# Kernel optimization log

Measured on AMD Instinct MI355X. Metric: run time of the kernel, lower is better.

## Reference

```python
import jax, jax.numpy as jnp
import numpy as np

B, N, H, NH = 2, 1024, 1024, 16  # batch, seq per branch, hidden, heads


def setup_inputs() -> dict:
    key = jax.random.key(0)
    k1, k2, k3, k4 = jax.random.split(key, 4)
    x = jax.random.normal(k1, (B, N, H), jnp.float32)
    x2 = jax.random.normal(k2, (B, N, H), jnp.float32)
    w_qkv = jax.random.normal(k3, (3 * H, H), jnp.float32) * 0.02  # nn.Linear(H, 3H), no bias
    w_out = jax.random.normal(k4, (H, H), jnp.float32) * 0.02
    b_out = jnp.zeros((H,), jnp.float32)
    return {"x": x, "x2": x2, "w_qkv": w_qkv, "w_out": w_out, "b_out": b_out, "num_heads": NH}


def _qkv_split(x, w_qkv, nh):
    # qkv Linear then Rearrange 'b n (qkv l d) -> qkv b l n d'
    b, n, h = x.shape
    d = h // nh
    qkv = x @ w_qkv.T                                    # [b, n, 3h]
    qkv = qkv.reshape(b, n, 3, nh, d).transpose(2, 0, 3, 1, 4)  # [3, b, nh, n, d]
    return qkv[0], qkv[1], qkv[2]


def reference(x, x2, w_qkv, w_out, b_out, num_heads):
    nh = num_heads
    d = x.shape[-1] // nh
    scale = float(d) ** -0.5
    q, k, v = _qkv_split(x, w_qkv, nh)
    q2, k2, v2 = _qkv_split(x2, w_qkv, nh)
    # cross-branch concat along seq dim
    q = jnp.concatenate([q, q2], axis=2)
    k = jnp.concatenate([k, k2], axis=2)
    v = jnp.concatenate([v, v2], axis=2)
    att = jax.nn.softmax(jnp.einsum('bhxd,bhyd->bhxy', q, k) * scale, axis=-1)  # [b,nh,2N,2N]
    o = jnp.einsum('bhxy,bhyd->bhxd', att, v)            # [b,nh,2N,d]
    o1, o2 = jnp.split(o, 2, axis=2)

    def proj(o):
        b, h, n, dd = o.shape
        o = o.transpose(0, 2, 1, 3).reshape(b, n, h * dd)  # 'b h l d -> b l (h d)'
        return o @ w_out.T + b_out

    return proj(o1), proj(o2)
```

## Files before the change

kernel.cpp:

```cpp
#include <hip/hip_runtime.h>
#include <hip/hip_bf16.h>

#define NB      2
#define NSEQ    1024
#define S2      2048
#define HDIM    1024
#define NHEADS  16
#define DHEAD   64
#define Q_SCALE 0.18033688011112042f

typedef unsigned short ushort_t;
typedef __attribute__((ext_vector_type(8))) short short8;
typedef __attribute__((ext_vector_type(4))) float f32x4;
typedef __attribute__((ext_vector_type(16))) float f32x16;

__device__ __forceinline__ ushort_t f2bf(float f) {
    union { float f; unsigned int u; } c; c.f = f;
    unsigned int u = c.u;
    u += 0x7FFFu + ((u >> 16) & 1u);
    return (ushort_t)(u >> 16);
}

__device__ __forceinline__ float bf2f(ushort_t u) {
    union { unsigned int u; float f; } c; c.u = ((unsigned int)u) << 16;
    return c.f;
}

__device__ __forceinline__ unsigned pack_bf16x2(float a, float b) {
    union { __hip_bfloat162 h; unsigned u; } cv;
    cv.h = __float22bfloat162_rn(float2{a, b});
    return cv.u;
}

__global__ __launch_bounds__(256) void cvt_all(
    const float* __restrict__ x, const float* __restrict__ x2,
    const float* __restrict__ wqkv, const float* __restrict__ wout,
    ushort_t* __restrict__ Xb, ushort_t* __restrict__ Wqb, ushort_t* __restrict__ Wob)
{
    int b = blockIdx.x;
    const float* s; ushort_t* d; int i;
    if (b < 2048)      { s = x;    d = Xb;            i = b * 256 + threadIdx.x; }
    else if (b < 4096) { s = x2;   d = Xb + 2097152;  i = (b - 2048) * 256 + threadIdx.x; }
    else if (b < 7168) { s = wqkv; d = Wqb;           i = (b - 4096) * 256 + threadIdx.x; }
    else               { s = wout; d = Wob;           i = (b - 7168) * 256 + threadIdx.x; }
    float4 v = ((const float4*)s)[i];
    ushort4 o; o.x = f2bf(v.x); o.y = f2bf(v.y); o.z = f2bf(v.z); o.w = f2bf(v.w);
    ((ushort4*)d)[i] = o;
}

__global__ __launch_bounds__(256) void qkv_gemm_mfma(
    const ushort_t* __restrict__ Xb, const ushort_t* __restrict__ Wqb,
    ushort_t* __restrict__ Qb, ushort_t* __restrict__ Kb, ushort_t* __restrict__ Vtb)
{
    __shared__ ushort_t As[2 * 128 * 32];
    __shared__ ushort_t Bs[2 * 128 * 32];
    const int t = threadIdx.x;
    const int lane = t & 63, quad = lane >> 4, l15 = lane & 15;
    const int w = t >> 6;
    const int wm = (w >> 1) * 64, wn = (w & 1) * 64;
    const int r0 = blockIdx.y * 128, c0 = blockIdx.x * 128;

    const int g_chunk = (lane & 3) ^ ((lane >> 3) & 3);
    const int srow_lo = w * 16 + (lane >> 2);

    auto stage = [&](int k0, int buf) {
        #pragma unroll
        for (int p = 0; p < 2; ++p) {
            int row = srow_lo + p * 64;
            const ushort_t* gpA = Xb  + (size_t)(r0 + row) * HDIM + k0 + g_chunk * 8;
            const ushort_t* gpB = Wqb + (size_t)(c0 + row) * HDIM + k0 + g_chunk * 8;
            ushort_t* lpA = As + buf * 4096 + p * 2048 + w * 512;
            ushort_t* lpB = Bs + buf * 4096 + p * 2048 + w * 512;
            __builtin_amdgcn_global_load_lds(
                (const __attribute__((address_space(1))) void*)gpA,
                (__attribute__((address_space(3))) void*)lpA, 16, 0, 0);
            __builtin_amdgcn_global_load_lds(
                (const __attribute__((address_space(1))) void*)gpB,
                (__attribute__((address_space(3))) void*)lpB, 16, 0, 0);
        }
    };

    f32x4 acc[4][4];
    #pragma unroll
    for (int i = 0; i < 4; ++i)
        #pragma unroll
        for (int j = 0; j < 4; ++j) acc[i][j] = (f32x4){0.f, 0.f, 0.f, 0.f};

    stage(0, 0);
    stage(32, 1);
    __syncthreads();

    const int sw = (l15 >> 1) & 3;
    for (int it = 0; it < 32; ++it) {
        const ushort_t* a = As + (it & 1) * 4096;
        const ushort_t* b = Bs + (it & 1) * 4096;
        short8 af[4], bf[4];
        #pragma unroll
        for (int mi = 0; mi < 4; ++mi) {
            int ra = wm + mi * 16 + l15;
            af[mi] = *(const short8*)(a + ra * 32 + ((quad ^ sw) * 8));
        }
        #pragma unroll
        for (int ni = 0; ni < 4; ++ni) {
            int rb = wn + ni * 16 + l15;
            bf[ni] = *(const short8*)(b + rb * 32 + ((quad ^ sw) * 8));
        }
        #pragma unroll
        for (int mi = 0; mi < 4; ++mi)
            #pragma unroll
            for (int ni = 0; ni < 4; ++ni)
                acc[mi][ni] = __builtin_amdgcn_mfma_f32_16x16x32_bf16(af[mi], bf[ni], acc[mi][ni], 0, 0, 0);
        __syncthreads();
        if (it < 30) stage((it + 2) * 32, it & 1);
    }

    const int branch = r0 >> 11;
    const int bb     = (r0 & 2047) >> 10;
    const int qi     = c0 >> 10;
    ushort_t* sq = As + w * 2048;
    const int erow = lane >> 2, ech = lane & 3;
    const int cc64 = (c0 & 1023) + wn;

    if (qi == 2) {
        const int sb64 = branch * NSEQ + (r0 & 1023) + wm;
        #pragma unroll
        for (int ni = 0; ni < 4; ++ni) {
            int cc = cc64 + ni * 16;
            int h = cc >> 6, dbase = cc & 63;
            #pragma unroll
            for (int mi = 0; mi < 4; ++mi)
                #pragma unroll
                for (int reg = 0; reg < 4; ++reg)
                    sq[l15 * 72 + mi * 16 + quad * 4 + reg] = f2bf(acc[mi][ni][reg]);
            short8 v0 = *(const short8*)(sq + erow * 72 + ech * 16);
            short8 v1 = *(const short8*)(sq + erow * 72 + ech * 16 + 8);
            ushort_t* dst = Vtb + ((size_t)(bb * NHEADS + h) * DHEAD + dbase + erow) * S2
                                + sb64 + ech * 16;
            *(short8*)dst = v0;
            *(short8*)(dst + 8) = v1;
        }
    } else {
        const float qsc = (qi == 0) ? Q_SCALE : 1.0f;
        ushort_t* base = (qi ? Kb : Qb);
        const int h = cc64 >> 6;
        #pragma unroll
        for (int mi = 0; mi < 4; ++mi) {
            int sb = branch * NSEQ + (r0 & 1023) + wm + mi * 16;
            #pragma unroll
            for (int ni = 0; ni < 4; ++ni)
                #pragma unroll
                for (int reg = 0; reg < 4; ++reg)
                    sq[(quad * 4 + reg) * 72 + ni * 16 + l15] = f2bf(acc[mi][ni][reg] * qsc);
            short8 v0 = *(const short8*)(sq + erow * 72 + ech * 16);
            short8 v1 = *(const short8*)(sq + erow * 72 + ech * 16 + 8);
            ushort_t* dst = base + ((size_t)(bb * NHEADS + h) * S2 + sb + erow) * DHEAD
                                 + ech * 16;
            *(short8*)dst = v0;
            *(short8*)(dst + 8) = v1;
        }
    }
}

__global__ __launch_bounds__(256, 4) void attn_mfma(
    const ushort_t* __restrict__ Qb, const ushort_t* __restrict__ Kb,
    const ushort_t* __restrict__ Vtb, ushort_t* __restrict__ Op0,
    ushort_t* __restrict__ Op1, float* __restrict__ Lp)
{
    __shared__ ushort_t Ks[2 * 64 * 64];
    __shared__ ushort_t Vs[2 * 64 * 64];

    const int t = threadIdx.x, lane = t & 63, w = t >> 6;
    const int l31 = lane & 31, hi = lane >> 5;

    const int id   = blockIdx.x;
    const int j    = id >> 3;
    const int bh   = ((j & 3) << 3) | (id & 7);
    const int j2   = j >> 2;
    const int r0   = (j2 & 15) << 7;
    const int half = j2 >> 4;
    const int kts  = half * 16;

    const ushort_t* Qh  = Qb  + (size_t)bh * S2 * DHEAD;
    const ushort_t* Kh  = Kb  + (size_t)bh * S2 * DHEAD;
    const ushort_t* Vth = Vtb + (size_t)bh * DHEAD * S2;

    const int slot = lane & 7;
    const int rsub = lane >> 3;
    auto prefetch = [&](int kt_, int buf_) {
        #pragma unroll
        for (int c = 0; c < 2; ++c) {
            int row = w * 16 + c * 8 + rsub;
            int g   = slot ^ (row & 7);
            const ushort_t* gpK = Kh  + (size_t)(kt_ * 64 + row) * DHEAD + g * 8;
            const ushort_t* gpV = Vth + (size_t)row * S2 + kt_ * 64 + g * 8;
            ushort_t* lpK = &Ks[buf_ * 4096 + w * 1024 + c * 512];
            ushort_t* lpV = &Vs[buf_ * 4096 + w * 1024 + c * 512];
            __builtin_amdgcn_global_load_lds(
                (const __attribute__((address_space(1))) void*)gpK,
                (__attribute__((address_space(3))) void*)lpK, 16, 0, 0);
            __builtin_amdgcn_global_load_lds(
                (const __attribute__((address_space(1))) void*)gpV,
                (__attribute__((address_space(3))) void*)lpV, 16, 0, 0);
        }
    };

    short8 aq[4];
    {
        const ushort_t* qp = Qh + (size_t)(r0 + 32 * w + l31) * DHEAD + hi * 8;
        #pragma unroll
        for (int sd = 0; sd < 4; ++sd) aq[sd] = *(const short8*)(qp + sd * 16);
    }

    const int s7 = l31 & 7;
    int offA[4];
    #pragma unroll
    for (int s = 0; s < 4; ++s)
        offA[s] = (l31 * 64 + (((s * 2 + hi) ^ s7) * 8)) * 2;

    f32x16 oacc0, oacc1;
    #pragma unroll
    for (int i = 0; i < 16; ++i) { oacc0[i] = 0.f; oacc1[i] = 0.f; }
    float la0 = 0.f, la1 = 0.f, la2 = 0.f, la3 = 0.f;

    prefetch(kts, 0);
    prefetch(kts + 1, 1);

    #pragma unroll 1
    for (int i = 0; i < 16; ++i) {
        if (i < 15) asm volatile("s_waitcnt vmcnt(4)" ::: "memory");
        else        asm volatile("s_waitcnt vmcnt(0)" ::: "memory");
        __builtin_amdgcn_s_barrier();
        __builtin_amdgcn_sched_barrier(0);

        const char* kb = (const char*)Ks + (i & 1) * 8192;
        const char* vb = (const char*)Vs + (i & 1) * 8192;

        f32x16 s0, s1;
        #pragma unroll
        for (int z = 0; z < 16; ++z) { s0[z] = 0.f; s1[z] = 0.f; }
        __builtin_amdgcn_s_setprio(1);
        #pragma unroll
        for (int sd = 0; sd < 4; ++sd) {
            short8 k0 = *(const short8*)(kb + offA[sd]);
            short8 k1 = *(const short8*)(kb + offA[sd] + 4096);
            s0 = __builtin_amdgcn_mfma_f32_32x32x16_bf16(k0, aq[sd], s0, 0, 0, 0);
            s1 = __builtin_amdgcn_mfma_f32_32x32x16_bf16(k1, aq[sd], s1, 0, 0, 0);
        }
        __builtin_amdgcn_s_setprio(0);

        unsigned pw[4][4];
        #pragma unroll
        for (int halfp = 0; halfp < 2; ++halfp) {
            float p[8], q[8];
            #pragma unroll
            for (int jj = 0; jj < 8; ++jj) {
                p[jj] = __builtin_exp2f(s0[halfp * 8 + jj]);
                q[jj] = __builtin_exp2f(s1[halfp * 8 + jj]);
            }
            la0 += p[0] + p[4]; la1 += p[1] + p[5];
            la2 += p[2] + p[6]; la3 += p[3] + p[7];
            la0 += q[0] + q[4]; la1 += q[1] + q[5];
            la2 += q[2] + q[6]; la3 += q[3] + q[7];

            unsigned a0 = pack_bf16x2(p[0], p[1]), b0 = pack_bf16x2(p[2], p[3]);
            unsigned c0_ = pack_bf16x2(p[4], p[5]), d0_ = pack_bf16x2(p[6], p[7]);
            asm("v_permlane32_swap_b32 %0, %1" : "+v"(a0), "+v"(c0_));
            asm("v_permlane32_swap_b32 %0, %1" : "+v"(b0), "+v"(d0_));
            pw[halfp][0] = a0; pw[halfp][1] = b0; pw[halfp][2] = c0_; pw[halfp][3] = d0_;

            unsigned a1 = pack_bf16x2(q[0], q[1]), b1 = pack_bf16x2(q[2], q[3]);
            unsigned c1_ = pack_bf16x2(q[4], q[5]), d1_ = pack_bf16x2(q[6], q[7]);
            asm("v_permlane32_swap_b32 %0, %1" : "+v"(a1), "+v"(c1_));
            asm("v_permlane32_swap_b32 %0, %1" : "+v"(b1), "+v"(d1_));
            pw[2 + halfp][0] = a1; pw[2 + halfp][1] = b1; pw[2 + halfp][2] = c1_; pw[2 + halfp][3] = d1_;
        }

        __builtin_amdgcn_s_setprio(1);
        #pragma unroll
        for (int sk = 0; sk < 4; ++sk) {
            union { unsigned u[4]; short8 s8; } pa;
            pa.u[0] = pw[sk][0]; pa.u[1] = pw[sk][1];
            pa.u[2] = pw[sk][2]; pa.u[3] = pw[sk][3];
            short8 v0 = *(const short8*)(vb + offA[sk]);
            short8 v1 = *(const short8*)(vb + offA[sk] + 4096);
            oacc0 = __builtin_amdgcn_mfma_f32_32x32x16_bf16(pa.s8, v0, oacc0, 0, 0, 0);
            oacc1 = __builtin_amdgcn_mfma_f32_32x32x16_bf16(pa.s8, v1, oacc1, 0, 0, 0);
        }
        __builtin_amdgcn_s_setprio(0);

        if (i <= 13) {
            __builtin_amdgcn_s_barrier();
            prefetch(kts + i + 2, i & 1);
        }
    }

    float l = (la0 + la1) + (la2 + la3);
    l += __shfl_xor(l, 32);
    const size_t rowb = (size_t)bh * S2 + r0 + 32 * w;
    if (hi == 0) Lp[(size_t)half * (32 * S2) + rowb + l31] = l;

    ushort_t* obase = (half ? Op1 : Op0) + rowb * DHEAD;
    #pragma unroll
    for (int r = 0; r < 16; ++r) {
        const int ql = (r & 3) + 8 * (r >> 2) + 4 * hi;
        const size_t rowoff = (size_t)ql * DHEAD;
        obase[rowoff + l31]      = f2bf(oacc0[r]);
        obase[rowoff + 32 + l31] = f2bf(oacc1[r]);
    }
}

__global__ __launch_bounds__(256) void combine_o(
    const ushort_t* __restrict__ Op1, const float* __restrict__ Lp,
    ushort_t* __restrict__ Ob )
{
    int idx = blockIdx.x * 256 + threadIdx.x;
    int e   = idx * 8;
    int row = e >> 6;
    float inv = 1.0f / (Lp[row] + Lp[32 * S2 + row]);
    union { short8 v; ushort_t u[8]; } a, b, o;
    a.v = *(const short8*)(Ob + e);
    b.v = *(const short8*)(Op1 + e);
    #pragma unroll
    for (int jj = 0; jj < 8; ++jj)
        o.u[jj] = f2bf((bf2f(a.u[jj]) + bf2f(b.u[jj])) * inv);
    *(short8*)(Ob + e) = o.v;
}

__global__ __launch_bounds__(256) void proj_gemm_mfma(
    const ushort_t* __restrict__ Ob, const ushort_t* __restrict__ Wob,
    const float* __restrict__ Bo, float* __restrict__ Out)
{
    __shared__ ushort_t As[2 * 128 * 32];
    __shared__ ushort_t Bs[2 * 64 * 32];
    __shared__ float    Sc[4][16 * 20];
    const int t = threadIdx.x;
    const int lane = t & 63, quad = lane >> 4, l15 = lane & 15;
    const int w = t >> 6;
    const int wm = (w >> 1) * 64, wn = (w & 1) * 32;
    const int r0 = blockIdx.y * 128, c0 = blockIdx.x * 64;
    const int branch = r0 >> 11, bb = (r0 & 2047) >> 10;

    const int g_chunk = (lane & 3) ^ ((lane >> 3) & 3);
    const int srow_lo = w * 16 + (lane >> 2);

    auto stage = [&](int k0, int buf) {
        int h = k0 >> 6, off = k0 & 63;
        const ushort_t* gpB = Wob + (size_t)(c0 + srow_lo) * HDIM + k0 + g_chunk * 8;
        ushort_t* lpB = Bs + buf * 2048 + w * 512;
        __builtin_amdgcn_global_load_lds(
            (const __attribute__((address_space(1))) void*)gpB,
            (__attribute__((address_space(3))) void*)lpB, 16, 0, 0);
        #pragma unroll
        for (int p = 0; p < 2; ++p) {
            int row = srow_lo + p * 64;
            int s = branch * NSEQ + (r0 & 1023) + row;
            const ushort_t* gpA = Ob + ((size_t)(bb * NHEADS + h) * S2 + s) * DHEAD + off + g_chunk * 8;
            ushort_t* lpA = As + buf * 4096 + p * 2048 + w * 512;
            __builtin_amdgcn_global_load_lds(
                (const __attribute__((address_space(1))) void*)gpA,
                (__attribute__((address_space(3))) void*)lpA, 16, 0, 0);
        }
    };

    f32x4 acc[4][2];
    #pragma unroll
    for (int i = 0; i < 4; ++i)
        #pragma unroll
        for (int j = 0; j < 2; ++j) acc[i][j] = (f32x4){0.f, 0.f, 0.f, 0.f};

    stage(0, 0);
    stage(32, 1);
    __syncthreads();

    const int sw = (l15 >> 1) & 3;
    for (int it = 0; it < 32; ++it) {
        const ushort_t* a = As + (it & 1) * 4096;
        const ushort_t* b = Bs + (it & 1) * 2048;
        short8 af[4], bf[2];
        #pragma unroll
        for (int mi = 0; mi < 4; ++mi) {
            int ra = wm + mi * 16 + l15;
            af[mi] = *(const short8*)(a + ra * 32 + ((quad ^ sw) * 8));
        }
        #pragma unroll
        for (int ni = 0; ni < 2; ++ni) {
            int rb = wn + ni * 16 + l15;
            bf[ni] = *(const short8*)(b + rb * 32 + ((quad ^ sw) * 8));
        }
        #pragma unroll
        for (int mi = 0; mi < 4; ++mi)
            #pragma unroll
            for (int ni = 0; ni < 2; ++ni)
                acc[mi][ni] = __builtin_amdgcn_mfma_f32_16x16x32_bf16(af[mi], bf[ni], acc[mi][ni], 0, 0, 0);
        __syncthreads();
        if (it < 30) stage((it + 2) * 32, it & 1);
    }

    float* sc = &Sc[w][0];
    const int row = lane >> 2, ch = lane & 3;
    #pragma unroll
    for (int mi = 0; mi < 4; ++mi) {
        int rb0 = r0 + wm + mi * 16;
        #pragma unroll
        for (int ni = 0; ni < 2; ++ni) {
            int cb = c0 + wn + ni * 16;
            #pragma unroll
            for (int reg = 0; reg < 4; ++reg)
                sc[(quad * 4 + reg) * 20 + l15] = acc[mi][ni][reg];
            float4 v = *(const float4*)&sc[row * 20 + ch * 4];
            float4 bias = *(const float4*)&Bo[cb + ch * 4];
            v.x += bias.x; v.y += bias.y; v.z += bias.z; v.w += bias.w;
            *(float4*)&Out[(size_t)(rb0 + row) * HDIM + cb + ch * 4] = v;
        }
    }
}

extern "C" void kernel_launch(void* const* d_in, const int* in_sizes, int n_in,
                              void* d_out, int out_size, void* d_ws, size_t ws_size,
                              hipStream_t stream) {
    const float* x    = (const float*)d_in[0];
    const float* x2   = (const float*)d_in[1];
    const float* wqkv = (const float*)d_in[2];
    const float* wout = (const float*)d_in[3];
    const float* bout = (const float*)d_in[4];
    float* out = (float*)d_out;

    char* ws = (char*)d_ws;
    ushort_t* Xb  = (ushort_t*)(ws);
    ushort_t* Wqb = (ushort_t*)(ws + (8u  << 20));
    ushort_t* Wob = (ushort_t*)(ws + (14u << 20));
    ushort_t* Qb  = (ushort_t*)(ws + (16u << 20));
    ushort_t* Kb  = (ushort_t*)(ws + (24u << 20));
    ushort_t* Vtb = (ushort_t*)(ws + (32u << 20));
    ushort_t* Op0 = (ushort_t*)(ws);
    float*    Lp  = (float*)   (ws + (8u  << 20));
    ushort_t* Op1 = (ushort_t*)(ws + (40u << 20));

    cvt_all<<<8192, 256, 0, stream>>>(x, x2, wqkv, wout, Xb, Wqb, Wob);
    qkv_gemm_mfma<<<dim3(24, 32), 256, 0, stream>>>(Xb, Wqb, Qb, Kb, Vtb);
    attn_mfma<<<1024, 256, 0, stream>>>(Qb, Kb, Vtb, Op0, Op1, Lp);
    combine_o<<<2048, 256, 0, stream>>>(Op1, Lp, Op0);
    proj_gemm_mfma<<<dim3(16, 32), 256, 0, stream>>>(Op0, Wob, bout, out);
}
```

Before: 202.2 us.

## Remap GEMM tiles per XCD and replace syncthreads with vmcnt-based waits

Both the QKV and projection GEMMs now use a 1D grid whose block index is remapped so that each XCD works on a contiguous 2D patch of tiles, which should improve L2 reuse of A and B panels. The main loop swaps the full __syncthreads for explicit s_waitcnt vmcnt counts plus raw s_barrier, so the next stage's global-to-LDS loads can stay in flight while the current tile is consumed. It also raises wave priority around the MFMA block. The risk is correctness if the vmcnt counts do not match the number of outstanding loads per stage.

```diff
diff --git a/kernel.cpp b/kernel.cpp
--- a/kernel.cpp
+++ b/kernel.cpp
@@ -58,7 +58,12 @@
     const int lane = t & 63, quad = lane >> 4, l15 = lane & 15;
     const int w = t >> 6;
     const int wm = (w >> 1) * 64, wn = (w & 1) * 64;
-    const int r0 = blockIdx.y * 128, c0 = blockIdx.x * 128;
+
+    const int id  = blockIdx.x;
+    const int xcd = id & 7, rr = id >> 3;
+    const int cxi = (xcd & 1) * 12 + (rr % 12);
+    const int ryi = (xcd >> 1) * 8 + (rr / 12);
+    const int r0 = ryi * 128, c0 = cxi * 128;
 
     const int g_chunk = (lane & 3) ^ ((lane >> 3) & 3);
     const int srow_lo = w * 16 + (lane >> 2);
@@ -88,10 +93,15 @@
 
     stage(0, 0);
     stage(32, 1);
-    __syncthreads();
 
     const int sw = (l15 >> 1) & 3;
+    #pragma unroll 1
     for (int it = 0; it < 32; ++it) {
+        if (it < 31) asm volatile("s_waitcnt vmcnt(4)" ::: "memory");
+        else         asm volatile("s_waitcnt vmcnt(0)" ::: "memory");
+        __builtin_amdgcn_s_barrier();
+        __builtin_amdgcn_sched_barrier(0);
+
         const ushort_t* a = As + (it & 1) * 4096;
         const ushort_t* b = Bs + (it & 1) * 4096;
         short8 af[4], bf[4];
@@ -105,14 +115,20 @@
             int rb = wn + ni * 16 + l15;
             bf[ni] = *(const short8*)(b + rb * 32 + ((quad ^ sw) * 8));
         }
+        __builtin_amdgcn_s_setprio(1);
         #pragma unroll
         for (int mi = 0; mi < 4; ++mi)
             #pragma unroll
             for (int ni = 0; ni < 4; ++ni)
                 acc[mi][ni] = __builtin_amdgcn_mfma_f32_16x16x32_bf16(af[mi], bf[ni], acc[mi][ni], 0, 0, 0);
-        __syncthreads();
-        if (it < 30) stage((it + 2) * 32, it & 1);
-    }
+        __builtin_amdgcn_s_setprio(0);
+
+        if (it <= 29) {
+            __builtin_amdgcn_s_barrier();
+            stage((it + 2) * 32, it & 1);
+        }
+    }
+    __syncthreads();
 
     const int branch = r0 >> 11;
     const int bb     = (r0 & 2047) >> 10;
@@ -337,7 +353,12 @@
     const int lane = t & 63, quad = lane >> 4, l15 = lane & 15;
     const int w = t >> 6;
     const int wm = (w >> 1) * 64, wn = (w & 1) * 32;
-    const int r0 = blockIdx.y * 128, c0 = blockIdx.x * 64;
+
+    const int id  = blockIdx.x;
+    const int xcd = id & 7, rr = id >> 3;
+    const int cxi = (xcd & 1) * 8 + (rr & 7);
+    const int ryi = (xcd >> 1) * 8 + (rr >> 3);
+    const int r0 = ryi * 128, c0 = cxi * 64;
     const int branch = r0 >> 11, bb = (r0 & 2047) >> 10;
 
     const int g_chunk = (lane & 3) ^ ((lane >> 3) & 3);
@@ -370,10 +391,15 @@
 
     stage(0, 0);
     stage(32, 1);
-    __syncthreads();
 
     const int sw = (l15 >> 1) & 3;
+    #pragma unroll 1
     for (int it = 0; it < 32; ++it) {
+        if (it < 31) asm volatile("s_waitcnt vmcnt(3)" ::: "memory");
+        else         asm volatile("s_waitcnt vmcnt(0)" ::: "memory");
+        __builtin_amdgcn_s_barrier();
+        __builtin_amdgcn_sched_barrier(0);
+
         const ushort_t* a = As + (it & 1) * 4096;
         const ushort_t* b = Bs + (it & 1) * 2048;
         short8 af[4], bf[2];
@@ -387,14 +413,20 @@
             int rb = wn + ni * 16 + l15;
             bf[ni] = *(const short8*)(b + rb * 32 + ((quad ^ sw) * 8));
         }
+        __builtin_amdgcn_s_setprio(1);
         #pragma unroll
         for (int mi = 0; mi < 4; ++mi)
             #pragma unroll
             for (int ni = 0; ni < 2; ++ni)
                 acc[mi][ni] = __builtin_amdgcn_mfma_f32_16x16x32_bf16(af[mi], bf[ni], acc[mi][ni], 0, 0, 0);
-        __syncthreads();
-        if (it < 30) stage((it + 2) * 32, it & 1);
-    }
+        __builtin_amdgcn_s_setprio(0);
+
+        if (it <= 29) {
+            __builtin_amdgcn_s_barrier();
+            stage((it + 2) * 32, it & 1);
+        }
+    }
+    __syncthreads();
 
     float* sc = &Sc[w][0];
     const int row = lane >> 2, ch = lane & 3;
@@ -437,8 +469,8 @@
     ushort_t* Op1 = (ushort_t*)(ws + (40u << 20));
 
     cvt_all<<<8192, 256, 0, stream>>>(x, x2, wqkv, wout, Xb, Wqb, Wob);
-    qkv_gemm_mfma<<<dim3(24, 32), 256, 0, stream>>>(Xb, Wqb, Qb, Kb, Vtb);
+    qkv_gemm_mfma<<<768, 256, 0, stream>>>(Xb, Wqb, Qb, Kb, Vtb);
     attn_mfma<<<1024, 256, 0, stream>>>(Qb, Kb, Vtb, Op0, Op1, Lp);
     combine_o<<<2048, 256, 0, stream>>>(Op1, Lp, Op0);
-    proj_gemm_mfma<<<dim3(16, 32), 256, 0, stream>>>(Op0, Wob, bout, out);
-}
+    proj_gemm_mfma<<<512, 256, 0, stream>>>(Op0, Wob, bout, out);
+}
```

Result: slower. 210.9 us (+4.3%).
